# Performance work log

Measured on AMD Instinct MI355X. Metric: run time of the kernel, lower is better.

The kernel has to match this reference:

```python
import jax, jax.numpy as jnp
import numpy as np

T, H, I, E, TOP_K = 2048, 1024, 768, 8, 2


def setup_inputs() -> dict:
    key = jax.random.key(0)
    kx, kg, ku, kd, kr = jax.random.split(key, 5)
    scale_h = 1.0 / np.sqrt(H)
    scale_i = 1.0 / np.sqrt(I)
    x = jax.random.normal(kx, (T, H), dtype=jnp.float32)
    gate_w = jax.random.normal(kg, (E, I, H), dtype=jnp.float32) * scale_h
    up_w = jax.random.normal(ku, (E, I, H), dtype=jnp.float32) * scale_h
    down_w = jax.random.normal(kd, (E, H, I), dtype=jnp.float32) * scale_i
    # Router: top-k over random logits, softmax over selected, scatter to dense [T, E]
    logits = jax.random.normal(kr, (T, E), dtype=jnp.float32)
    top_vals, top_idx = jax.lax.top_k(logits, TOP_K)          # [T, K]
    top_w = jax.nn.softmax(top_vals, axis=-1)                 # [T, K]
    rows = jnp.arange(T)[:, None]                             # [T, 1]
    masked_routing_weights = jnp.zeros((T, E), jnp.float32).at[rows, top_idx].set(top_w)
    expert_select_count = jnp.zeros((E,), jnp.int32).at[top_idx.reshape(-1)].add(1)
    return {
        "x": x,
        "gate_w": gate_w,
        "up_w": up_w,
        "down_w": down_w,
        "masked_routing_weights": masked_routing_weights,
        "expert_select_count": expert_select_count,
    }


def reference(x, gate_w, up_w, down_w, masked_routing_weights, expert_select_count):
    # custom_moe_glu: per-expert GLU MLP, combined with masked routing weights.
    # x: [T, H]; gate_w/up_w: [E, I, H]; down_w: [E, H, I]; routing: [T, E]
    g = jnp.einsum("th,eih->tei", x, gate_w)                  # [T, E, I]
    u = jnp.einsum("th,eih->tei", x, up_w)                    # [T, E, I]
    h = jax.nn.silu(g) * u                                    # fused GLU activation
    # down projection per expert, then weighted combine over experts
    out = jnp.einsum("tei,ehi,te->th", h, down_w, masked_routing_weights)
    return out
```

## Files before the change

kernel.cpp:

```cpp
#include <hip/hip_runtime.h>
#include <hip/hip_bf16.h>

#define T_TOK 2048
#define H_DIM 1024
#define I_DIM 768
#define NEXP  8
#define WPE   6291456

typedef short bf16x8  __attribute__((ext_vector_type(8)));
typedef short short4v __attribute__((ext_vector_type(4)));
typedef float f32x4   __attribute__((ext_vector_type(4)));

__device__ __forceinline__ short f2bf(float f) {
  __bf16 b = (__bf16)f;
  return __builtin_bit_cast(short, b);
}
__device__ __forceinline__ void gload16(const void* g, void* l) {
  __builtin_amdgcn_global_load_lds(
      (const __attribute__((address_space(1))) void*)g,
      (__attribute__((address_space(3))) void*)l, 16, 0, 0);
}
__device__ __forceinline__ int padcnt(int c) { return (c + 127) & ~127; }
__device__ __forceinline__ int ebase(const int* __restrict__ cnts, int e) {
  int b = 0;
#pragma unroll
  for (int i = 0; i < NEXP; ++i)
    if (i < e) b += padcnt(cnts[i]);
  return b;
}


__global__ __launch_bounds__(512) void prep(const float* __restrict__ routw,
                                            const float* __restrict__ gw,
                                            const float* __restrict__ uw,
                                            const float* __restrict__ dw,
                                            unsigned short* __restrict__ wbf,
                                            float* __restrict__ out,
                                            int* __restrict__ wsI) {
  int bid = blockIdx.x, tid = threadIdx.x;
  if (bid < 8) {
    __shared__ int sc[8];
    int e = bid, lane = tid & 63, w = tid >> 6;
    unsigned long long mk[4];
    int cnt = 0;
#pragma unroll
    for (int c = 0; c < 4; ++c) {
      int tk = w * 256 + c * 64 + lane;
      float v = routw[(size_t)tk * NEXP + e];
      mk[c] = __ballot(v > 0.f);
      cnt += __popcll(mk[c]);
    }
    if (lane == 0) sc[w] = cnt;
    __syncthreads();
    int pre = 0;
#pragma unroll
    for (int j = 0; j < 8; ++j)
      if (j < w) pre += sc[j];
    int run = pre;
#pragma unroll
    for (int c = 0; c < 4; ++c) {
      int tk = w * 256 + c * 64 + lane;
      if ((mk[c] >> lane) & 1ull) {
        int pos = __popcll(mk[c] & ((1ull << lane) - 1));
        wsI[64 + e * T_TOK + run + pos] = tk;
      }
      run += __popcll(mk[c]);
    }
    if (w == 7 && lane == 0) wsI[e] = run;
  } else if (bid < 1032) {
    int i = (bid - 8) * 512 + tid;
    f32x4 z = {0.f, 0.f, 0.f, 0.f};
    *(f32x4*)(out + (size_t)i * 4) = z;
  } else {
    int gid = (bid - 1032) * 512 + tid;
    int a = gid / 393216;
    int rem = (gid - a * 393216) * 16;
    const float* s = (a == 0) ? gw : (a == 1) ? uw : dw;
    unsigned short* o = wbf + (size_t)a * WPE + rem;
#pragma unroll
    for (int j = 0; j < 4; ++j) {
      float4 v = *(const float4*)(s + rem + j * 4);
      short4v b = {f2bf(v.x), f2bf(v.y), f2bf(v.z), f2bf(v.w)};
      *(short4v*)(o + j * 4) = b;
    }
  }
}

__global__ __launch_bounds__(256) void xgather(const float* __restrict__ x,
                                               const int* __restrict__ wsI,
                                               unsigned short* __restrict__ xc) {
  int e = blockIdx.x >> 9;
  int rb = blockIdx.x & 511;
  int cnt = wsI[e];
  int pad = padcnt(cnt);
  int r = rb * 4 + (threadIdx.x >> 6);
  if (r >= pad) return;
  int base = ebase(wsI, e);
  int col = (threadIdx.x & 63) * 16;
  unsigned short* dst = xc + (size_t)(base + r) * H_DIM + col;
  if (r < cnt) {
    int tok = wsI[64 + e * T_TOK + r];
    const float* sr = x + (size_t)tok * H_DIM + col;
#pragma unroll
    for (int j = 0; j < 4; ++j) {
      float4 v = *(const float4*)(sr + j * 4);
      short4v b = {f2bf(v.x), f2bf(v.y), f2bf(v.z), f2bf(v.w)};
      *(short4v*)(dst + j * 4) = b;
    }
  } else {
#pragma unroll
    for (int j = 0; j < 4; ++j) {
      short4v z = {0, 0, 0, 0};
      *(short4v*)(dst + j * 4) = z;
    }
  }
}

__global__ __launch_bounds__(512, 2) void moe_gemm1(
    const unsigned short* __restrict__ xc, const unsigned short* __restrict__ wbf,
    const int* __restrict__ wsI, unsigned short* __restrict__ h) {
  int e = blockIdx.x & 7, rr = blockIdx.x >> 3;
  int mt = rr & 15, nt = rr >> 4;
  int cnt = wsI[e];
  int m0 = mt * 128;
  if (m0 >= cnt) return;
  int base = ebase(wsI, e);
  int n0 = nt * 128;

  __shared__ unsigned short ls[2][24576];

  int tid = threadIdx.x, lane = tid & 63, w = tid >> 6;
  int wm = w >> 2, wn = w & 3;
  int fr = lane & 15, fg = lane >> 4;

  const unsigned short* gate_bf = wbf;
  const unsigned short* up_bf   = wbf + WPE;

  int srow = lane >> 2;
  int scol = ((lane & 3) ^ (srow & 3)) * 8;
  const unsigned short* srcA = xc + (size_t)(base + m0 + 16 * w + srow) * H_DIM + scol;
  const unsigned short* srcG = gate_bf + (size_t)(e * I_DIM + n0 + 16 * w + srow) * H_DIM + scol;
  const unsigned short* srcU = up_bf   + (size_t)(e * I_DIM + n0 + 16 * w + srow) * H_DIM + scol;
  const int ldA = w * 512;
  const int ldG = 8192 + w * 512;
  const int ldU = 12288 + w * 512;

  int offA[2][4], offB[2][4];
#pragma unroll
  for (int kh = 0; kh < 2; ++kh) {
#pragma unroll
    for (int m = 0; m < 4; ++m) {
      int row = wm * 64 + m * 16 + fr;
      offA[kh][m] = kh * 4096 + row * 32 + ((fg ^ (row & 3)) << 3);
    }
#pragma unroll
    for (int jn = 0; jn < 4; ++jn) {
      int brow = (jn < 2) ? (wn * 32 + jn * 16 + fr) : (128 + wn * 32 + (jn - 2) * 16 + fr);
      offB[kh][jn] = 8192 + kh * 8192 + brow * 32 + ((fg ^ (brow & 3)) << 3);
    }
  }

  f32x4 acc[4][4] = {};

#define STG1(buf, t, kh)                                            \
  do {                                                              \
    gload16(srcA + (t) * 64 + (kh) * 32, &ls[buf][ldA + (kh) * 4096]); \
    gload16(srcG + (t) * 64 + (kh) * 32, &ls[buf][ldG + (kh) * 8192]); \
    gload16(srcU + (t) * 64 + (kh) * 32, &ls[buf][ldU + (kh) * 8192]); \
  } while (0)

  STG1(0, 0, 0);
  STG1(0, 0, 1);
  asm volatile("s_waitcnt vmcnt(3)" ::: "memory");
  __builtin_amdgcn_s_barrier();

  for (int t = 0; t < 16; ++t) {
    int cb = t & 1;
    if (t + 1 < 16) STG1(cb ^ 1, t + 1, 0);
    {
      bf16x8 af[4], bf[4];
#pragma unroll
      for (int m = 0; m < 4; ++m) af[m] = *(const bf16x8*)&ls[cb][offA[0][m]];
#pragma unroll
      for (int jn = 0; jn < 4; ++jn) bf[jn] = *(const bf16x8*)&ls[cb][offB[0][jn]];
#pragma unroll
      for (int m = 0; m < 4; ++m)
#pragma unroll
        for (int jn = 0; jn < 4; ++jn)
          acc[m][jn] = __builtin_amdgcn_mfma_f32_16x16x32_bf16(af[m], bf[jn], acc[m][jn], 0, 0, 0);
    }
    if (t + 1 < 16) asm volatile("s_waitcnt vmcnt(3)" ::: "memory");
    else            asm volatile("s_waitcnt vmcnt(0)" ::: "memory");
    __builtin_amdgcn_s_barrier();
    if (t + 1 < 16) STG1(cb ^ 1, t + 1, 1);
    {
      bf16x8 af[4], bf[4];
#pragma unroll
      for (int m = 0; m < 4; ++m) af[m] = *(const bf16x8*)&ls[cb][offA[1][m]];
#pragma unroll
      for (int jn = 0; jn < 4; ++jn) bf[jn] = *(const bf16x8*)&ls[cb][offB[1][jn]];
#pragma unroll
      for (int m = 0; m < 4; ++m)
#pragma unroll
        for (int jn = 0; jn < 4; ++jn)
          acc[m][jn] = __builtin_amdgcn_mfma_f32_16x16x32_bf16(af[m], bf[jn], acc[m][jn], 0, 0, 0);
    }
    if (t + 1 < 16) asm volatile("s_waitcnt vmcnt(3)" ::: "memory");
    else            asm volatile("s_waitcnt vmcnt(0)" ::: "memory");
    __builtin_amdgcn_s_barrier();
  }
#undef STG1

#pragma unroll
  for (int m = 0; m < 4; ++m)
#pragma unroll
    for (int j = 0; j < 4; ++j) {
      int row = wm * 64 + m * 16 + fg * 4 + j;
      size_t rb2 = (size_t)(base + m0 + row) * I_DIM + n0;
#pragma unroll
      for (int jn = 0; jn < 2; ++jn) {
        float g = acc[m][jn][j];
        float u = acc[m][jn + 2][j];
        h[rb2 + wn * 32 + jn * 16 + fr] = (unsigned short)f2bf(g * u / (1.f + __expf(-g)));
      }
    }
}

__global__ __launch_bounds__(256, 2) void moe_gemm2(
    const unsigned short* __restrict__ h, const unsigned short* __restrict__ wbf,
    const int* __restrict__ wsI, const float* __restrict__ routw,
    float* __restrict__ out) {
  int e = blockIdx.x & 7, rr = blockIdx.x >> 3;
  int mt = rr & 15, nt = rr >> 4;
  int cnt = wsI[e];
  int m0 = mt * 128;
  if (m0 >= cnt) return;
  int base = ebase(wsI, e);
  int n0 = nt * 128;
  const unsigned short* down_bf = wbf + 2 * WPE;

  __shared__ unsigned short ls[2][16384];

  int tid = threadIdx.x, lane = tid & 63, w = tid >> 6;
  int wm = w >> 1, wn = w & 1;
  int fr = lane & 15, fg = lane >> 4;

  int srow = lane >> 2;
  int scol = ((lane & 3) ^ (srow & 3)) * 8;
  const unsigned short* srcA1 = h + (size_t)(base + m0 + 16 * w + srow) * I_DIM + scol;
  const unsigned short* srcA2 = h + (size_t)(base + m0 + 16 * (w + 4) + srow) * I_DIM + scol;
  const unsigned short* srcB1 = down_bf + (size_t)(e * H_DIM + n0 + 16 * w + srow) * I_DIM + scol;
  const unsigned short* srcB2 = down_bf + (size_t)(e * H_DIM + n0 + 16 * (w + 4) + srow) * I_DIM + scol;
  const int ldA1 = w * 512;
  const int ldA2 = (w + 4) * 512;
  const int ldB1 = 8192 + w * 512;
  const int ldB2 = 8192 + (w + 4) * 512;

  int offA[2][4], offB[2][4];
#pragma unroll
  for (int kh = 0; kh < 2; ++kh) {
#pragma unroll
    for (int m = 0; m < 4; ++m) {
      int row = wm * 64 + m * 16 + fr;
      offA[kh][m] = kh * 4096 + row * 32 + ((fg ^ (row & 3)) << 3);
    }
#pragma unroll
    for (int n = 0; n < 4; ++n) {
      int row = wn * 64 + n * 16 + fr;
      offB[kh][n] = 8192 + kh * 4096 + row * 32 + ((fg ^ (row & 3)) << 3);
    }
  }

  f32x4 acc[4][4] = {};

#define STG2(buf, t, kh)                                               \
  do {                                                                 \
    gload16(srcA1 + (t) * 64 + (kh) * 32, &ls[buf][ldA1 + (kh) * 4096]); \
    gload16(srcA2 + (t) * 64 + (kh) * 32, &ls[buf][ldA2 + (kh) * 4096]); \
    gload16(srcB1 + (t) * 64 + (kh) * 32, &ls[buf][ldB1 + (kh) * 4096]); \
    gload16(srcB2 + (t) * 64 + (kh) * 32, &ls[buf][ldB2 + (kh) * 4096]); \
  } while (0)

  STG2(0, 0, 0);
  STG2(0, 0, 1);
  asm volatile("s_waitcnt vmcnt(4)" ::: "memory");
  __builtin_amdgcn_s_barrier();

  for (int t = 0; t < 12; ++t) {
    int cb = t & 1;
    if (t + 1 < 12) STG2(cb ^ 1, t + 1, 0);
    {
      bf16x8 af[4], bf[4];
#pragma unroll
      for (int m = 0; m < 4; ++m) af[m] = *(const bf16x8*)&ls[cb][offA[0][m]];
#pragma unroll
      for (int n = 0; n < 4; ++n) bf[n] = *(const bf16x8*)&ls[cb][offB[0][n]];
#pragma unroll
      for (int m = 0; m < 4; ++m)
#pragma unroll
        for (int n = 0; n < 4; ++n)
          acc[m][n] = __builtin_amdgcn_mfma_f32_16x16x32_bf16(af[m], bf[n], acc[m][n], 0, 0, 0);
    }
    if (t + 1 < 12) asm volatile("s_waitcnt vmcnt(4)" ::: "memory");
    else            asm volatile("s_waitcnt vmcnt(0)" ::: "memory");
    __builtin_amdgcn_s_barrier();
    if (t + 1 < 12) STG2(cb ^ 1, t + 1, 1);
    {
      bf16x8 af[4], bf[4];
#pragma unroll
      for (int m = 0; m < 4; ++m) af[m] = *(const bf16x8*)&ls[cb][offA[1][m]];
#pragma unroll
      for (int n = 0; n < 4; ++n) bf[n] = *(const bf16x8*)&ls[cb][offB[1][n]];
#pragma unroll
      for (int m = 0; m < 4; ++m)
#pragma unroll
        for (int n = 0; n < 4; ++n)
          acc[m][n] = __builtin_amdgcn_mfma_f32_16x16x32_bf16(af[m], bf[n], acc[m][n], 0, 0, 0);
    }
    if (t + 1 < 12) asm volatile("s_waitcnt vmcnt(4)" ::: "memory");
    else            asm volatile("s_waitcnt vmcnt(0)" ::: "memory");
    __builtin_amdgcn_s_barrier();
  }
#undef STG2

#pragma unroll
  for (int m = 0; m < 4; ++m)
#pragma unroll
    for (int j = 0; j < 4; ++j) {
      int row = wm * 64 + m * 16 + fg * 4 + j;
      int grow = m0 + row;
      if (grow < cnt) {
        int tk = wsI[64 + e * T_TOK + grow];
        float rw = routw[(size_t)tk * NEXP + e];
        float* orow = out + (size_t)tk * H_DIM + n0 + wn * 64;
#pragma unroll
        for (int n = 0; n < 4; ++n)
          atomicAdd(orow + n * 16 + fr, acc[m][n][j] * rw);
      }
    }
}

extern "C" void kernel_launch(void* const* d_in, const int* in_sizes, int n_in,
                              void* d_out, int out_size, void* d_ws, size_t ws_size,
                              hipStream_t stream) {
  const float* x      = (const float*)d_in[0];
  const float* gate_w = (const float*)d_in[1];
  const float* up_w   = (const float*)d_in[2];
  const float* down_w = (const float*)d_in[3];
  const float* routw  = (const float*)d_in[4];
  float* out = (float*)d_out;
  int* wsI = (int*)d_ws;

  unsigned short* wbf = (unsigned short*)((char*)d_ws + 131072);
  unsigned short* xc  = (unsigned short*)((char*)d_ws + 37879808);
  unsigned short* h   = (unsigned short*)((char*)d_ws + 48365568);

  prep<<<3336, 512, 0, stream>>>(routw, gate_w, up_w, down_w, wbf, out, wsI);
  xgather<<<4096, 256, 0, stream>>>(x, wsI, xc);
  moe_gemm1<<<768, 512, 0, stream>>>(xc, wbf, wsI, h);
  moe_gemm2<<<1024, 256, 0, stream>>>(h, wbf, wsI, routw, out);
}
```

Measured before the change: 92.09 us.

## Restructure MoE pipeline: deeper LDS ring buffers, register double-buffering, overlapped conversion work

```diff
diff --git a/kernel.cpp b/kernel.cpp
--- a/kernel.cpp
+++ b/kernel.cpp
@@ -30,96 +30,116 @@
 }
 
 
-__global__ __launch_bounds__(512) void prep(const float* __restrict__ routw,
-                                            const float* __restrict__ gw,
-                                            const float* __restrict__ uw,
-                                            const float* __restrict__ dw,
-                                            unsigned short* __restrict__ wbf,
-                                            float* __restrict__ out,
-                                            int* __restrict__ wsI) {
-  int bid = blockIdx.x, tid = threadIdx.x;
-  if (bid < 8) {
-    __shared__ int sc[8];
-    int e = bid, lane = tid & 63, w = tid >> 6;
-    unsigned long long mk[4];
-    int cnt = 0;
-#pragma unroll
-    for (int c = 0; c < 4; ++c) {
-      int tk = w * 256 + c * 64 + lane;
-      float v = routw[(size_t)tk * NEXP + e];
-      mk[c] = __ballot(v > 0.f);
-      cnt += __popcll(mk[c]);
-    }
-    if (lane == 0) sc[w] = cnt;
-    __syncthreads();
-    int pre = 0;
-#pragma unroll
-    for (int j = 0; j < 8; ++j)
-      if (j < w) pre += sc[j];
-    int run = pre;
-#pragma unroll
-    for (int c = 0; c < 4; ++c) {
-      int tk = w * 256 + c * 64 + lane;
-      if ((mk[c] >> lane) & 1ull) {
-        int pos = __popcll(mk[c] & ((1ull << lane) - 1));
-        wsI[64 + e * T_TOK + run + pos] = tk;
-      }
-      run += __popcll(mk[c]);
-    }
-    if (w == 7 && lane == 0) wsI[e] = run;
-  } else if (bid < 1032) {
-    int i = (bid - 8) * 512 + tid;
-    f32x4 z = {0.f, 0.f, 0.f, 0.f};
-    *(f32x4*)(out + (size_t)i * 4) = z;
+__global__ __launch_bounds__(512) void compact_k(const float* __restrict__ routw,
+                                                 int* __restrict__ wsI) {
+  __shared__ int sc[8];
+  int e = blockIdx.x, lane = threadIdx.x & 63, w = threadIdx.x >> 6;
+  unsigned long long mk[4];
+  int cnt = 0;
+#pragma unroll
+  for (int c = 0; c < 4; ++c) {
+    int tk = w * 256 + c * 64 + lane;
+    float v = routw[(size_t)tk * NEXP + e];
+    mk[c] = __ballot(v > 0.f);
+    cnt += __popcll(mk[c]);
+  }
+  if (lane == 0) sc[w] = cnt;
+  __syncthreads();
+  int run = 0;
+#pragma unroll
+  for (int j = 0; j < 8; ++j)
+    if (j < w) run += sc[j];
+#pragma unroll
+  for (int c = 0; c < 4; ++c) {
+    int tk = w * 256 + c * 64 + lane;
+    if ((mk[c] >> lane) & 1ull) {
+      int pos = __popcll(mk[c] & ((1ull << lane) - 1));
+      wsI[64 + e * T_TOK + run + pos] = tk;
+    }
+    run += __popcll(mk[c]);
+  }
+  if (w == 7 && lane == 0) wsI[e] = run;
+}
+
+__global__ __launch_bounds__(256) void gatherconv_k(const float* __restrict__ x,
+                                                    const float* __restrict__ gw,
+                                                    const float* __restrict__ uw,
+                                                    const int* __restrict__ wsI,
+                                                    unsigned short* __restrict__ xc,
+                                                    unsigned short* __restrict__ wbf) {
+  int bid = blockIdx.x;
+  if (bid < 4096) {
+    int e = bid >> 9, rb = bid & 511;
+    int cnt = wsI[e];
+    int pad = padcnt(cnt);
+    int r = rb * 4 + (threadIdx.x >> 6);
+    if (r >= pad) return;
+    int base = ebase(wsI, e);
+    int col = (threadIdx.x & 63) * 16;
+    unsigned short* dst = xc + (size_t)(base + r) * H_DIM + col;
+    if (r < cnt) {
+      int tok = wsI[64 + e * T_TOK + r];
+      const float* sr = x + (size_t)tok * H_DIM + col;
+#pragma unroll
+      for (int j = 0; j < 4; ++j) {
+        float4 v = *(const float4*)(sr + j * 4);
+        short4v b = {f2bf(v.x), f2bf(v.y), f2bf(v.z), f2bf(v.w)};
+        *(short4v*)(dst + j * 4) = b;
+      }
+    } else {
+#pragma unroll
+      for (int j = 0; j < 4; ++j) {
+        short4v z = {0, 0, 0, 0};
+        *(short4v*)(dst + j * 4) = z;
+      }
+    }
   } else {
-    int gid = (bid - 1032) * 512 + tid;
-    int a = gid / 393216;
-    int rem = (gid - a * 393216) * 16;
-    const float* s = (a == 0) ? gw : (a == 1) ? uw : dw;
+    size_t off = ((size_t)(bid - 4096) * 256 + threadIdx.x) * 16;
+    int a = (off >= (size_t)WPE) ? 1 : 0;
+    size_t rem = off - (size_t)a * WPE;
+    const float* s = (a ? uw : gw) + rem;
     unsigned short* o = wbf + (size_t)a * WPE + rem;
 #pragma unroll
     for (int j = 0; j < 4; ++j) {
-      float4 v = *(const float4*)(s + rem + j * 4);
+      float4 v = *(const float4*)(s + j * 4);
       short4v b = {f2bf(v.x), f2bf(v.y), f2bf(v.z), f2bf(v.w)};
       *(short4v*)(o + j * 4) = b;
     }
   }
 }
 
-__global__ __launch_bounds__(256) void xgather(const float* __restrict__ x,
-                                               const int* __restrict__ wsI,
-                                               unsigned short* __restrict__ xc) {
-  int e = blockIdx.x >> 9;
-  int rb = blockIdx.x & 511;
-  int cnt = wsI[e];
-  int pad = padcnt(cnt);
-  int r = rb * 4 + (threadIdx.x >> 6);
-  if (r >= pad) return;
-  int base = ebase(wsI, e);
-  int col = (threadIdx.x & 63) * 16;
-  unsigned short* dst = xc + (size_t)(base + r) * H_DIM + col;
-  if (r < cnt) {
-    int tok = wsI[64 + e * T_TOK + r];
-    const float* sr = x + (size_t)tok * H_DIM + col;
-#pragma unroll
-    for (int j = 0; j < 4; ++j) {
-      float4 v = *(const float4*)(sr + j * 4);
-      short4v b = {f2bf(v.x), f2bf(v.y), f2bf(v.z), f2bf(v.w)};
-      *(short4v*)(dst + j * 4) = b;
-    }
-  } else {
-#pragma unroll
-    for (int j = 0; j < 4; ++j) {
-      short4v z = {0, 0, 0, 0};
-      *(short4v*)(dst + j * 4) = z;
-    }
-  }
-}
-
-__global__ __launch_bounds__(512, 2) void moe_gemm1(
-    const unsigned short* __restrict__ xc, const unsigned short* __restrict__ wbf,
-    const int* __restrict__ wsI, unsigned short* __restrict__ h) {
-  int e = blockIdx.x & 7, rr = blockIdx.x >> 3;
+#define WB(v)                                              \
+  do {                                                     \
+    asm volatile("s_waitcnt vmcnt(" #v ")" ::: "memory");  \
+    __builtin_amdgcn_s_barrier();                          \
+    __builtin_amdgcn_sched_barrier(0);                     \
+  } while (0)
+
+__global__ __launch_bounds__(512, 2) void gemm1_k(
+    const unsigned short* __restrict__ xc, unsigned short* __restrict__ wbf,
+    const int* __restrict__ wsI, unsigned short* __restrict__ h,
+    const float* __restrict__ dw, float* __restrict__ out) {
+  int bid = blockIdx.x;
+  if (bid >= 768) {
+    if (bid < 1536) {
+      size_t off = ((size_t)(bid - 768) * 512 + threadIdx.x) * 16;
+      const float* s = dw + off;
+      unsigned short* o = wbf + 2 * (size_t)WPE + off;
+#pragma unroll
+      for (int j = 0; j < 4; ++j) {
+        float4 v = *(const float4*)(s + j * 4);
+        short4v b = {f2bf(v.x), f2bf(v.y), f2bf(v.z), f2bf(v.w)};
+        *(short4v*)(o + j * 4) = b;
+      }
+    } else {
+      size_t off = ((size_t)(bid - 1536) * 512 + threadIdx.x) * 16;
+      f32x4 z = {0.f, 0.f, 0.f, 0.f};
+#pragma unroll
+      for (int j = 0; j < 4; ++j) *(f32x4*)(out + off + j * 4) = z;
+    }
+    return;
+  }
+  int e = bid & 7, rr = bid >> 3;
   int mt = rr & 15, nt = rr >> 4;
   int cnt = wsI[e];
   int m0 = mt * 128;
@@ -127,89 +147,70 @@
   int base = ebase(wsI, e);
   int n0 = nt * 128;
 
-  __shared__ unsigned short ls[2][24576];
+  __shared__ unsigned short ls[5][12288];
 
   int tid = threadIdx.x, lane = tid & 63, w = tid >> 6;
   int wm = w >> 2, wn = w & 3;
   int fr = lane & 15, fg = lane >> 4;
-
-  const unsigned short* gate_bf = wbf;
-  const unsigned short* up_bf   = wbf + WPE;
-
   int srow = lane >> 2;
   int scol = ((lane & 3) ^ (srow & 3)) * 8;
+
   const unsigned short* srcA = xc + (size_t)(base + m0 + 16 * w + srow) * H_DIM + scol;
-  const unsigned short* srcG = gate_bf + (size_t)(e * I_DIM + n0 + 16 * w + srow) * H_DIM + scol;
-  const unsigned short* srcU = up_bf   + (size_t)(e * I_DIM + n0 + 16 * w + srow) * H_DIM + scol;
-  const int ldA = w * 512;
-  const int ldG = 8192 + w * 512;
-  const int ldU = 12288 + w * 512;
-
-  int offA[2][4], offB[2][4];
-#pragma unroll
-  for (int kh = 0; kh < 2; ++kh) {
-#pragma unroll
-    for (int m = 0; m < 4; ++m) {
-      int row = wm * 64 + m * 16 + fr;
-      offA[kh][m] = kh * 4096 + row * 32 + ((fg ^ (row & 3)) << 3);
-    }
-#pragma unroll
-    for (int jn = 0; jn < 4; ++jn) {
-      int brow = (jn < 2) ? (wn * 32 + jn * 16 + fr) : (128 + wn * 32 + (jn - 2) * 16 + fr);
-      offB[kh][jn] = 8192 + kh * 8192 + brow * 32 + ((fg ^ (brow & 3)) << 3);
-    }
-  }
-
+  const unsigned short* srcG = wbf + (size_t)(e * I_DIM + n0 + 16 * w + srow) * H_DIM + scol;
+  const unsigned short* srcU = wbf + WPE + (size_t)(e * I_DIM + n0 + 16 * w + srow) * H_DIM + scol;
+
+  int roA[4], roB[4];
+#pragma unroll
+  for (int m = 0; m < 4; ++m) {
+    int r2 = wm * 64 + m * 16 + fr;
+    roA[m] = r2 * 32 + ((fg ^ (r2 & 3)) << 3);
+  }
+#pragma unroll
+  for (int n = 0; n < 4; ++n) {
+    int r2 = (n < 2) ? (wn * 32 + n * 16 + fr) : (128 + wn * 32 + (n - 2) * 16 + fr);
+    roB[n] = 4096 + r2 * 32 + ((fg ^ (r2 & 3)) << 3);
+  }
+
+  bf16x8 af[2][4], bv[2][4];
   f32x4 acc[4][4] = {};
 
-#define STG1(buf, t, kh)                                            \
-  do {                                                              \
-    gload16(srcA + (t) * 64 + (kh) * 32, &ls[buf][ldA + (kh) * 4096]); \
-    gload16(srcG + (t) * 64 + (kh) * 32, &ls[buf][ldG + (kh) * 8192]); \
-    gload16(srcU + (t) * 64 + (kh) * 32, &ls[buf][ldU + (kh) * 8192]); \
-  } while (0)
-
-  STG1(0, 0, 0);
-  STG1(0, 0, 1);
-  asm volatile("s_waitcnt vmcnt(3)" ::: "memory");
-  __builtin_amdgcn_s_barrier();
-
-  for (int t = 0; t < 16; ++t) {
-    int cb = t & 1;
-    if (t + 1 < 16) STG1(cb ^ 1, t + 1, 0);
-    {
-      bf16x8 af[4], bf[4];
-#pragma unroll
-      for (int m = 0; m < 4; ++m) af[m] = *(const bf16x8*)&ls[cb][offA[0][m]];
-#pragma unroll
-      for (int jn = 0; jn < 4; ++jn) bf[jn] = *(const bf16x8*)&ls[cb][offB[0][jn]];
-#pragma unroll
-      for (int m = 0; m < 4; ++m)
-#pragma unroll
-        for (int jn = 0; jn < 4; ++jn)
-          acc[m][jn] = __builtin_amdgcn_mfma_f32_16x16x32_bf16(af[m], bf[jn], acc[m][jn], 0, 0, 0);
-    }
-    if (t + 1 < 16) asm volatile("s_waitcnt vmcnt(3)" ::: "memory");
-    else            asm volatile("s_waitcnt vmcnt(0)" ::: "memory");
-    __builtin_amdgcn_s_barrier();
-    if (t + 1 < 16) STG1(cb ^ 1, t + 1, 1);
-    {
-      bf16x8 af[4], bf[4];
-#pragma unroll
-      for (int m = 0; m < 4; ++m) af[m] = *(const bf16x8*)&ls[cb][offA[1][m]];
-#pragma unroll
-      for (int jn = 0; jn < 4; ++jn) bf[jn] = *(const bf16x8*)&ls[cb][offB[1][jn]];
-#pragma unroll
-      for (int m = 0; m < 4; ++m)
-#pragma unroll
-        for (int jn = 0; jn < 4; ++jn)
-          acc[m][jn] = __builtin_amdgcn_mfma_f32_16x16x32_bf16(af[m], bf[jn], acc[m][jn], 0, 0, 0);
-    }
-    if (t + 1 < 16) asm volatile("s_waitcnt vmcnt(3)" ::: "memory");
-    else            asm volatile("s_waitcnt vmcnt(0)" ::: "memory");
-    __builtin_amdgcn_s_barrier();
+#define STG1(hh)                                                     \
+  do {                                                               \
+    unsigned short* lb = &ls[(hh) % 5][0];                           \
+    gload16(srcA + (hh) * 32, lb + w * 512);                         \
+    gload16(srcG + (hh) * 32, lb + 4096 + w * 512);                  \
+    gload16(srcU + (hh) * 32, lb + 4096 + (w + 8) * 512);            \
+  } while (0)
+#define LDF1(st, hh)                                                 \
+  do {                                                               \
+    const unsigned short* lb = &ls[(hh) % 5][0];                     \
+    _Pragma("unroll") for (int m = 0; m < 4; ++m) af[st][m] = *(const bf16x8*)(lb + roA[m]); \
+    _Pragma("unroll") for (int n = 0; n < 4; ++n) bv[st][n] = *(const bf16x8*)(lb + roB[n]); \
+  } while (0)
+#define MM1(st)                                                      \
+  do {                                                               \
+    __builtin_amdgcn_s_setprio(1);                                   \
+    _Pragma("unroll") for (int m = 0; m < 4; ++m)                    \
+      _Pragma("unroll") for (int n = 0; n < 4; ++n)                  \
+        acc[m][n] = __builtin_amdgcn_mfma_f32_16x16x32_bf16(af[st][m], bv[st][n], acc[m][n], 0, 0, 0); \
+    __builtin_amdgcn_s_setprio(0);                                   \
+  } while (0)
+
+  STG1(0); STG1(1); STG1(2); STG1(3);
+  WB(6);
+  LDF1(0, 0);
+#pragma unroll
+  for (int i = 0; i < 32; ++i) {
+    if (i + 4 < 32) STG1(i + 4);
+    if (i + 1 < 32) LDF1((i + 1) & 1, i + 1);
+    MM1(i & 1);
+    if (i <= 27)      WB(6);
+    else if (i == 28) WB(3);
+    else if (i == 29) WB(0);
   }
 #undef STG1
+#undef LDF1
+#undef MM1
 
 #pragma unroll
   for (int m = 0; m < 4; ++m)
@@ -226,7 +227,7 @@
     }
 }
 
-__global__ __launch_bounds__(256, 2) void moe_gemm2(
+__global__ __launch_bounds__(512, 2) void gemm2_k(
     const unsigned short* __restrict__ h, const unsigned short* __restrict__ wbf,
     const int* __restrict__ wsI, const float* __restrict__ routw,
     float* __restrict__ out) {
@@ -236,92 +237,73 @@
   int m0 = mt * 128;
   if (m0 >= cnt) return;
   int base = ebase(wsI, e);
-  int n0 = nt * 128;
-  const unsigned short* down_bf = wbf + 2 * WPE;
-
-  __shared__ unsigned short ls[2][16384];
+  int n0 = nt * 256;
+  const unsigned short* down_bf = wbf + 2 * (size_t)WPE;
+
+  __shared__ unsigned short ls[5][12288];
 
   int tid = threadIdx.x, lane = tid & 63, w = tid >> 6;
-  int wm = w >> 1, wn = w & 1;
+  int wm = w >> 2, wn = w & 3;
   int fr = lane & 15, fg = lane >> 4;
-
   int srow = lane >> 2;
   int scol = ((lane & 3) ^ (srow & 3)) * 8;
-  const unsigned short* srcA1 = h + (size_t)(base + m0 + 16 * w + srow) * I_DIM + scol;
-  const unsigned short* srcA2 = h + (size_t)(base + m0 + 16 * (w + 4) + srow) * I_DIM + scol;
+
+  const unsigned short* srcA  = h + (size_t)(base + m0 + 16 * w + srow) * I_DIM + scol;
   const unsigned short* srcB1 = down_bf + (size_t)(e * H_DIM + n0 + 16 * w + srow) * I_DIM + scol;
-  const unsigned short* srcB2 = down_bf + (size_t)(e * H_DIM + n0 + 16 * (w + 4) + srow) * I_DIM + scol;
-  const int ldA1 = w * 512;
-  const int ldA2 = (w + 4) * 512;
-  const int ldB1 = 8192 + w * 512;
-  const int ldB2 = 8192 + (w + 4) * 512;
-
-  int offA[2][4], offB[2][4];
-#pragma unroll
-  for (int kh = 0; kh < 2; ++kh) {
-#pragma unroll
-    for (int m = 0; m < 4; ++m) {
-      int row = wm * 64 + m * 16 + fr;
-      offA[kh][m] = kh * 4096 + row * 32 + ((fg ^ (row & 3)) << 3);
-    }
-#pragma unroll
-    for (int n = 0; n < 4; ++n) {
-      int row = wn * 64 + n * 16 + fr;
-      offB[kh][n] = 8192 + kh * 4096 + row * 32 + ((fg ^ (row & 3)) << 3);
-    }
-  }
-
+  const unsigned short* srcB2 = down_bf + (size_t)(e * H_DIM + n0 + 16 * (w + 8) + srow) * I_DIM + scol;
+
+  int roA[4], roB[4];
+#pragma unroll
+  for (int m = 0; m < 4; ++m) {
+    int r2 = wm * 64 + m * 16 + fr;
+    roA[m] = r2 * 32 + ((fg ^ (r2 & 3)) << 3);
+  }
+#pragma unroll
+  for (int n = 0; n < 4; ++n) {
+    int r2 = wn * 64 + n * 16 + fr;
+    roB[n] = 4096 + r2 * 32 + ((fg ^ (r2 & 3)) << 3);
+  }
+
+  bf16x8 af[2][4], bv[2][4];
   f32x4 acc[4][4] = {};
 
-#define STG2(buf, t, kh)                                               \
-  do {                                                                 \
-    gload16(srcA1 + (t) * 64 + (kh) * 32, &ls[buf][ldA1 + (kh) * 4096]); \
-    gload16(srcA2 + (t) * 64 + (kh) * 32, &ls[buf][ldA2 + (kh) * 4096]); \
-    gload16(srcB1 + (t) * 64 + (kh) * 32, &ls[buf][ldB1 + (kh) * 4096]); \
-    gload16(srcB2 + (t) * 64 + (kh) * 32, &ls[buf][ldB2 + (kh) * 4096]); \
-  } while (0)
-
-  STG2(0, 0, 0);
-  STG2(0, 0, 1);
-  asm volatile("s_waitcnt vmcnt(4)" ::: "memory");
-  __builtin_amdgcn_s_barrier();
-
-  for (int t = 0; t < 12; ++t) {
-    int cb = t & 1;
-    if (t + 1 < 12) STG2(cb ^ 1, t + 1, 0);
-    {
-      bf16x8 af[4], bf[4];
-#pragma unroll
-      for (int m = 0; m < 4; ++m) af[m] = *(const bf16x8*)&ls[cb][offA[0][m]];
-#pragma unroll
-      for (int n = 0; n < 4; ++n) bf[n] = *(const bf16x8*)&ls[cb][offB[0][n]];
-#pragma unroll
-      for (int m = 0; m < 4; ++m)
-#pragma unroll
-        for (int n = 0; n < 4; ++n)
-          acc[m][n] = __builtin_amdgcn_mfma_f32_16x16x32_bf16(af[m], bf[n], acc[m][n], 0, 0, 0);
-    }
-    if (t + 1 < 12) asm volatile("s_waitcnt vmcnt(4)" ::: "memory");
-    else            asm volatile("s_waitcnt vmcnt(0)" ::: "memory");
-    __builtin_amdgcn_s_barrier();
-    if (t + 1 < 12) STG2(cb ^ 1, t + 1, 1);
-    {
-      bf16x8 af[4], bf[4];
-#pragma unroll
-      for (int m = 0; m < 4; ++m) af[m] = *(const bf16x8*)&ls[cb][offA[1][m]];
-#pragma unroll
-      for (int n = 0; n < 4; ++n) bf[n] = *(const bf16x8*)&ls[cb][offB[1][n]];
-#pragma unroll
-      for (int m = 0; m < 4; ++m)
-#pragma unroll
-        for (int n = 0; n < 4; ++n)
-          acc[m][n] = __builtin_amdgcn_mfma_f32_16x16x32_bf16(af[m], bf[n], acc[m][n], 0, 0, 0);
-    }
-    if (t + 1 < 12) asm volatile("s_waitcnt vmcnt(4)" ::: "memory");
-    else            asm volatile("s_waitcnt vmcnt(0)" ::: "memory");
-    __builtin_amdgcn_s_barrier();
+#define STG2(hh)                                                     \
+  do {                                                               \
+    unsigned short* lb = &ls[(hh) % 5][0];                           \
+    gload16(srcA + (hh) * 32, lb + w * 512);                         \
+    gload16(srcB1 + (hh) * 32, lb + 4096 + w * 512);                 \
+    gload16(srcB2 + (hh) * 32, lb + 4096 + (w + 8) * 512);           \
+  } while (0)
+#define LDF2(st, hh)                                                 \
+  do {                                                               \
+    const unsigned short* lb = &ls[(hh) % 5][0];                     \
+    _Pragma("unroll") for (int m = 0; m < 4; ++m) af[st][m] = *(const bf16x8*)(lb + roA[m]); \
+    _Pragma("unroll") for (int n = 0; n < 4; ++n) bv[st][n] = *(const bf16x8*)(lb + roB[n]); \
+  } while (0)
+#define MM2(st)                                                      \
+  do {                                                               \
+    __builtin_amdgcn_s_setprio(1);                                   \
+    _Pragma("unroll") for (int m = 0; m < 4; ++m)                    \
+      _Pragma("unroll") for (int n = 0; n < 4; ++n)                  \
+        acc[m][n] = __builtin_amdgcn_mfma_f32_16x16x32_bf16(af[st][m], bv[st][n], acc[m][n], 0, 0, 0); \
+    __builtin_amdgcn_s_setprio(0);                                   \
+  } while (0)
+
+  STG2(0); STG2(1); STG2(2); STG2(3);
+  WB(6);
+  LDF2(0, 0);
+#pragma unroll
+  for (int i = 0; i < 24; ++i) {
+    if (i + 4 < 24) STG2(i + 4);
+    if (i + 1 < 24) LDF2((i + 1) & 1, i + 1);
+    MM2(i & 1);
+    if (i <= 19)      WB(6);
+    else if (i == 20) WB(3);
+    else if (i == 21) WB(0);
   }
 #undef STG2
+#undef LDF2
+#undef MM2
 
 #pragma unroll
   for (int m = 0; m < 4; ++m)
@@ -355,8 +337,8 @@
   unsigned short* xc  = (unsigned short*)((char*)d_ws + 37879808);
   unsigned short* h   = (unsigned short*)((char*)d_ws + 48365568);
 
-  prep<<<3336, 512, 0, stream>>>(routw, gate_w, up_w, down_w, wbf, out, wsI);
-  xgather<<<4096, 256, 0, stream>>>(x, wsI, xc);
-  moe_gemm1<<<768, 512, 0, stream>>>(xc, wbf, wsI, h);
-  moe_gemm2<<<1024, 256, 0, stream>>>(h, wbf, wsI, routw, out);
-}
+  compact_k<<<8, 512, 0, stream>>>(routw, wsI);
+  gatherconv_k<<<7168, 256, 0, stream>>>(x, gate_w, up_w, wsI, xc, wbf);
+  gemm1_k<<<1792, 512, 0, stream>>>(xc, wbf, wsI, h, down_w, out);
+  gemm2_k<<<512, 512, 0, stream>>>(h, wbf, wsI, routw, out);
+}
```

New measurement: 87.19 us. 5.3% less time.
